# Kernel tuning notes

Hardware: AMD Instinct MI355X
Metric: run time of the kernel (lower is better)

Reference implementation:

```python
import jax, jax.numpy as jnp
import numpy as np

PS = 16            # patch size
STEP = PS - 2      # stride (overlap of 2)
HEADS = 4
DIM = 64
QK = 64
MLP = 128

def _grid(h):
    # static (numpy) row indices of all patch pixels, matching patch_divide's loop
    starts = np.arange(0, h + STEP - PS, STEP)
    tops = np.minimum(starts + PS, h) - PS
    return (tops[:, None] + np.arange(PS)).ravel(), len(starts)

def _div_mask(h):
    # rows/cols covered by two patches get divided by 2 (patch_reverse loops)
    m = np.ones(h, np.float32)
    for i in range(STEP, h + STEP - PS, STEP):
        d = min(i + PS - STEP, h)
        if i < d:
            m[i:d] = 2.0
    return m

def _layernorm(x, g, b):
    mu = x.mean(-1, keepdims=True)
    var = ((x - mu) ** 2).mean(-1, keepdims=True)
    return (x - mu) * jax.lax.rsqrt(var + 1e-5) * g + b

def setup_inputs() -> dict:
    key = jax.random.key(0)
    ks = jax.random.split(key, 8)
    f = lambda k, shp: jax.random.normal(k, shp, jnp.float32) * 0.05
    return {
        "x": jax.random.normal(ks[0], (2, DIM, 226, 226), jnp.float32),
        "ln1_g": jnp.ones((DIM,), jnp.float32), "ln1_b": jnp.zeros((DIM,), jnp.float32),
        "wq": f(ks[1], (DIM, QK)), "wk": f(ks[2], (DIM, QK)), "wv": f(ks[3], (DIM, DIM)),
        "w_proj": f(ks[4], (DIM, DIM)), "b_proj": jnp.zeros((DIM,), jnp.float32),
        "ln2_g": jnp.ones((DIM,), jnp.float32), "ln2_b": jnp.zeros((DIM,), jnp.float32),
        "w_fc1": f(ks[5], (DIM, MLP)), "b_fc1": jnp.zeros((MLP,), jnp.float32),
        "w_dw": f(ks[6], (MLP, 1, 5, 5)), "b_dw": jnp.zeros((MLP,), jnp.float32),
        "w_fc2": f(ks[7], (MLP, DIM)), "b_fc2": jnp.zeros((DIM,), jnp.float32),
    }

def reference(x, ln1_g, ln1_b, wq, wk, wv, w_proj, b_proj,
              ln2_g, ln2_b, w_fc1, b_fc1, w_dw, b_dw, w_fc2, b_fc2):
    b, c, h, w = x.shape
    ri, nh = _grid(h)
    ci, nw = _grid(w)
    n = nh * nw
    # --- patch_divide (vectorized gather of overlapping windows) ---
    p = x[:, :, ri][:, :, :, ci].reshape(b, c, nh, PS, nw, PS)
    t = p.transpose(0, 2, 4, 3, 5, 1).reshape(b * n, PS * PS, c)  # (b n)(h w)c
    # --- PreNorm attention (SDPA default scale = head_dim**-0.5) ---
    y = _layernorm(t, ln1_g, ln1_b)
    dh = QK // HEADS
    q = (y @ wq).reshape(-1, PS * PS, HEADS, dh)
    k = (y @ wk).reshape(-1, PS * PS, HEADS, dh)
    v = (y @ wv).reshape(-1, PS * PS, HEADS, DIM // HEADS)
    logits = jnp.einsum('bqhd,bkhd->bhqk', q, k) * (dh ** -0.5)
    a = jax.nn.softmax(logits, axis=-1)
    o = jnp.einsum('bhqk,bkhd->bqhd', a, v).reshape(-1, PS * PS, DIM)
    t = (o @ w_proj + b_proj) + t
    # --- PreNorm ConvFFN ---
    y = _layernorm(t, ln2_g, ln2_b)
    y = jax.nn.gelu(y @ w_fc1 + b_fc1, approximate=False)
    img = y.reshape(-1, PS, PS, MLP).transpose(0, 3, 1, 2)  # NCHW
    dw = jax.lax.conv_general_dilated(
        img, w_dw, (1, 1), [(2, 2), (2, 2)],
        feature_group_count=MLP,
        dimension_numbers=('NCHW', 'OIHW', 'NCHW')) + b_dw[None, :, None, None]
    dw = jax.nn.gelu(dw, approximate=False).transpose(0, 2, 3, 1).reshape(y.shape)
    y = y + dw
    t = (y @ w_fc2 + b_fc2) + t
    # --- patch_reverse (overlap-add scatter + averaging of double-covered bands) ---
    vals = t.reshape(b, nh, nw, PS, PS, c).transpose(0, 5, 1, 3, 2, 4).reshape(b, c, -1)
    idx = (ri[:, None] * w + ci[None, :]).ravel()
    out = jnp.zeros((b, c, h * w), x.dtype).at[:, :, idx].add(vals)
    out = out.reshape(b, c, h, w) / (_div_mask(h)[:, None] * _div_mask(w)[None, :])
    return out
```

## Files before the change

### kernel.cpp

```cpp
#include <hip/hip_runtime.h>
#include <hip/hip_bf16.h>
#include <math.h>

#define HH 226
#define WW 226
#define HWIMG (226*226)
#define PS 16
#define STP 14
#define TOK 256
#define NPATCH 512
#define NTOK (NPATCH*TOK)
#define OUT_ELEMS (2*64*226*226)

typedef unsigned int u32;
typedef unsigned short u16;
typedef __attribute__((ext_vector_type(8))) short short8;
typedef __attribute__((ext_vector_type(4))) float f32x4;

__device__ __forceinline__ float lo16(u32 u){ return __uint_as_float(u << 16); }
__device__ __forceinline__ float hi16(u32 u){ return __uint_as_float(u & 0xFFFF0000u); }
__device__ __forceinline__ u16 f2bf(float f){
    u32 u = __float_as_uint(f);
    u += 0x7FFFu + ((u >> 16) & 1u);
    return (u16)(u >> 16);
}
__device__ __forceinline__ u32 pack2(float a, float b){
#if defined(__gfx950__) && __has_builtin(__builtin_amdgcn_cvt_pk_bf16_f32)
    auto r = __builtin_amdgcn_cvt_pk_bf16_f32(a, b);
    return *(u32*)&r;
#else
    return (u32)f2bf(a) | ((u32)f2bf(b) << 16);
#endif
}
__device__ __forceinline__ float fexp2(float x){
#if __has_builtin(__builtin_amdgcn_exp2f)
    return __builtin_amdgcn_exp2f(x);
#else
    return exp2f(x);
#endif
}
__device__ __forceinline__ void unpack8(uint4 r, float* d){
    d[0]=lo16(r.x); d[1]=hi16(r.x); d[2]=lo16(r.y); d[3]=hi16(r.y);
    d[4]=lo16(r.z); d[5]=hi16(r.z); d[6]=lo16(r.w); d[7]=hi16(r.w);
}
__device__ __forceinline__ uint4 pack8(const float* a){
    uint4 uu;
    uu.x = pack2(a[0], a[1]);
    uu.y = pack2(a[2], a[3]);
    uu.z = pack2(a[4], a[5]);
    uu.w = pack2(a[6], a[7]);
    return uu;
}
__device__ __forceinline__ float gelu_f(float x){
    return 0.5f * x * (1.0f + erff(x * 0.70710678118654752f));
}

template<int N>
__device__ __forceinline__ void store_bf16(u32* dst, const float* a){
    uint4* p4 = (uint4*)(dst);
    #pragma unroll
    for (int w4 = 0; w4 < N/8; ++w4) p4[w4] = pack8(a + 8*w4);
}

__global__ __launch_bounds__(256, 4) void k0_wt(
    const float* __restrict__ wq, const float* __restrict__ wk,
    const float* __restrict__ wv, u16* __restrict__ wt)
{
    const int i = blockIdx.x*256 + threadIdx.x;
    const int m = i >> 12, rem = i & 4095;
    const int kk = rem >> 6, n = rem & 63;
    const float* w = (m==0 ? wq : (m==1 ? wk : wv));
    wt[m*4096 + n*64 + kk] = f2bf(w[kk*64 + n]);
}

__global__ __launch_bounds__(512, 4) void k1_qkv(
    const float* __restrict__ x, const float* __restrict__ g1, const float* __restrict__ b1,
    const u16* __restrict__ wt,
    float* __restrict__ t_out, u32* __restrict__ qo, u32* __restrict__ ko, u32* __restrict__ vo)
{
    __shared__ u16 ys[256*72];
    __shared__ u32 strip[8][16*34];
    __shared__ float g_s[64], b_s[64];
    const int tid = threadIdx.x;
    if (tid < 64){ g_s[tid]=g1[tid]; b_s[tid]=b1[tid]; }

    const int p = blockIdx.x;
    const int bi = p >> 8, ph = (p >> 4) & 15, pw = p & 15;

    const int tok = tid >> 1, h = tid & 1;
    const int ti = tok >> 4, tj = tok & 15;
    const int r = ph*STP + ti, c = pw*STP + tj;
    const float* xb = x + ((size_t)bi*64 + 32*h)*HWIMG + (size_t)r*WW + c;
    const size_t gtokA = (size_t)p*TOK + tok;
    float* tp = t_out + gtokA*64 + 32*h;

    float v32[32];
    float s1 = 0.f, s2 = 0.f;
    #pragma unroll
    for (int c8 = 0; c8 < 4; ++c8){
        #pragma unroll
        for (int u = 0; u < 8; ++u){
            const float vv = xb[(size_t)(c8*8+u)*HWIMG];
            v32[c8*8+u] = vv;
            s1 += vv; s2 += vv*vv;
        }
        ((float4*)tp)[c8*2]   = make_float4(v32[c8*8+0],v32[c8*8+1],v32[c8*8+2],v32[c8*8+3]);
        ((float4*)tp)[c8*2+1] = make_float4(v32[c8*8+4],v32[c8*8+5],v32[c8*8+6],v32[c8*8+7]);
    }
    s1 += __shfl_xor(s1, 1);
    s2 += __shfl_xor(s2, 1);
    const float mu = s1 * (1.f/64.f);
    const float var = s2 * (1.f/64.f) - mu*mu;
    const float rs = rsqrtf(var + 1e-5f);
    __syncthreads();
    u32* ysw = (u32*)ys;
    #pragma unroll
    for (int i2 = 0; i2 < 16; ++i2){
        const int kk = 32*h + 2*i2;
        const float a0 = (v32[2*i2]  -mu)*rs*g_s[kk]   + b_s[kk];
        const float a1 = (v32[2*i2+1]-mu)*rs*g_s[kk+1] + b_s[kk+1];
        ysw[tok*36 + 16*h + i2] = pack2(a0, a1);
    }
    __syncthreads();

    const int lane = tid & 63;
    const int w8   = tid >> 6;
    const int c15  = lane & 15;
    const int quad = lane >> 4;
    u32* stw = strip[w8];
    const size_t ptok = (size_t)p * TOK;

    for (int mt = 0; mt < 2; ++mt){
        const int T = w8*32 + mt*16;
        short8 af[2];
        #pragma unroll
        for (int kb = 0; kb < 2; ++kb)
            af[kb] = *(const short8*)(ys + (T + c15)*72 + kb*32 + quad*8);

        #pragma unroll
        for (int m = 0; m < 3; ++m){
            short8 bf[2][4];
            #pragma unroll
            for (int kb = 0; kb < 2; ++kb)
                #pragma unroll
                for (int nt = 0; nt < 4; ++nt)
                    bf[kb][nt] = *(const short8*)(wt + m*4096 + (nt*16 + c15)*64 + kb*32 + quad*8);

            f32x4 C[4];
            #pragma unroll
            for (int nt = 0; nt < 4; ++nt) C[nt] = (f32x4){0.f,0.f,0.f,0.f};
            #pragma unroll
            for (int kb = 0; kb < 2; ++kb)
                #pragma unroll
                for (int nt = 0; nt < 4; ++nt)
                    C[nt] = __builtin_amdgcn_mfma_f32_16x16x32_bf16(af[kb], bf[kb][nt], C[nt], 0, 0, 0);

            if (m == 0){
                #pragma unroll
                for (int nt = 0; nt < 4; ++nt)
                    #pragma unroll
                    for (int rr = 0; rr < 4; ++rr)
                        C[nt][rr] *= 0.3606737602222409f;
            }

            #pragma unroll
            for (int nt = 0; nt < 4; ++nt){
                #pragma unroll
                for (int r2 = 0; r2 < 2; ++r2){
                    const float pv0 = __shfl_xor(C[nt][2*r2],   1);
                    const float pv1 = __shfl_xor(C[nt][2*r2+1], 1);
                    u32 wrd; int row;
                    if ((lane & 1) == 0){ wrd = pack2(C[nt][2*r2], pv0);  row = quad*4 + 2*r2; }
                    else                { wrd = pack2(pv1, C[nt][2*r2+1]); row = quad*4 + 2*r2 + 1; }
                    stw[row*34 + nt*8 + (c15 >> 1)] = wrd;
                }
            }

            u32* om = (m==0 ? qo : (m==1 ? ko : vo));
            #pragma unroll
            for (int i = 0; i < 8; ++i){
                const int flat = i*64 + lane;
                const u32 wv = stw[(flat >> 5)*34 + (flat & 31)];
                om[(ptok + T)*32 + flat] = wv;
            }
        }
    }
}

__global__ __launch_bounds__(256, 2) void k2_attn(
    const u16* __restrict__ qg, const u16* __restrict__ kg,
    const u16* __restrict__ vg, u16* __restrict__ og)
{
    __shared__ u16 plds[4][16*280];
    const int tid  = threadIdx.x;
    const int lane = tid & 63;
    const int h    = tid >> 6;
    const int pb   = blockIdx.x;
    const int p    = pb >> 1;
    const int half = pb & 1;
    const int c15  = lane & 15;
    const int quad = lane >> 4;
    const size_t pbase = (size_t)p * TOK * 64;

    short8 kf[16];
    #pragma unroll
    for (int t = 0; t < 16; ++t){
        short8 bf = {0,0,0,0,0,0,0,0};
        if (quad < 2)
            bf = *(const short8*)(kg + pbase + (size_t)(t*16 + c15)*64 + h*16 + quad*8);
        kf[t] = bf;
    }
    short8 vf[8];
    #pragma unroll
    for (int kb = 0; kb < 8; ++kb){
        #pragma unroll
        for (int j = 0; j < 8; ++j)
            vf[kb][j] = (short)vg[pbase + (size_t)(kb*32 + quad*8 + j)*64 + h*16 + c15];
    }
    u16* pw  = &plds[h][0];
    u32* pwq = (u32*)pw + c15*140;

    for (int qi = 0; qi < 8; ++qi){
        const int qt = half*8 + qi;

        short8 qf = {0,0,0,0,0,0,0,0};
        if (quad < 2)
            qf = *(const short8*)(qg + pbase + (size_t)(qt*16 + c15)*64 + h*16 + quad*8);

        f32x4 St[16];
        #pragma unroll
        for (int t = 0; t < 16; ++t){
            f32x4 z = {0.f,0.f,0.f,0.f};
            St[t] = __builtin_amdgcn_mfma_f32_16x16x32_bf16(kf[t], qf, z, 0, 0, 0);
        }

        float rsm[4] = {0.f,0.f,0.f,0.f};
        #pragma unroll
        for (int t = 0; t < 16; ++t){
            #pragma unroll
            for (int r = 0; r < 4; ++r){
                const float pe = fexp2(St[t][r]);
                St[t][r] = pe;
                rsm[r] += pe;
            }
        }
        float s = (rsm[0]+rsm[1]) + (rsm[2]+rsm[3]);
        s += __shfl_xor(s, 16);
        s += __shfl_xor(s, 32);
        const float rinv = __builtin_amdgcn_rcpf(s);
        float rv[4];
        #pragma unroll
        for (int r = 0; r < 4; ++r) rv[r] = __shfl(rinv, quad*4 + r);

        #pragma unroll
        for (int t = 0; t < 16; ++t){
            uint2 wr;
            wr.x = pack2(St[t][0], St[t][1]);
            wr.y = pack2(St[t][2], St[t][3]);
            *(uint2*)(pwq + t*8 + quad*2) = wr;
        }

        f32x4 O0 = {0.f,0.f,0.f,0.f}, O1 = {0.f,0.f,0.f,0.f};
        #pragma unroll
        for (int kb = 0; kb < 4; ++kb){
            const short8 a0 = *(const short8*)(pw + c15*280 + (2*kb)*32 + quad*8);
            const short8 a1 = *(const short8*)(pw + c15*280 + (2*kb+1)*32 + quad*8);
            O0 = __builtin_amdgcn_mfma_f32_16x16x32_bf16(a0, vf[2*kb],   O0, 0, 0, 0);
            O1 = __builtin_amdgcn_mfma_f32_16x16x32_bf16(a1, vf[2*kb+1], O1, 0, 0, 0);
        }

        #pragma unroll
        for (int r = 0; r < 4; ++r){
            const float ov = (O0[r] + O1[r]) * rv[r];
            og[pbase + (size_t)(qt*16 + quad*4 + r)*64 + h*16 + c15] = f2bf(ov);
        }
    }
}

__global__ __launch_bounds__(256, 2) void k3_proj_fc1(
    const u16* __restrict__ og, float* __restrict__ t,
    const float* __restrict__ wp, const float* __restrict__ bp,
    const float* __restrict__ g2, const float* __restrict__ b2,
    const float* __restrict__ wf1, const float* __restrict__ bf1,
    u32* __restrict__ y3)
{
    __shared__ u16 strip[4][16*136];
    __shared__ float bp_s[64], g_s[64], b_s[64], bf_s[128];
    const int tid  = threadIdx.x;
    const int lane = tid & 63;
    const int w    = tid >> 6;
    const int c15  = lane & 15;
    const int quad = lane >> 4;
    if (tid < 64){ bp_s[tid]=bp[tid]; g_s[tid]=g2[tid]; b_s[tid]=b2[tid]; }
    else if (tid >= 128){ const int j = tid - 128; bf_s[j] = bf1[j]; }
    __syncthreads();

    short8 wpf[2][4];
    short8 wff[2][8];
    #pragma unroll
    for (int kb = 0; kb < 2; ++kb){
        #pragma unroll
        for (int nt = 0; nt < 4; ++nt){
            #pragma unroll
            for (int j = 0; j < 8; ++j)
                wpf[kb][nt][j] = (short)f2bf(wp[(kb*32 + quad*8 + j)*64 + nt*16 + c15]);
        }
        #pragma unroll
        for (int nt = 0; nt < 8; ++nt){
            #pragma unroll
            for (int j = 0; j < 8; ++j)
                wff[kb][nt][j] = (short)f2bf(wf1[(kb*32 + quad*8 + j)*128 + nt*16 + c15]);
        }
    }

    const int p = blockIdx.x;
    const size_t pbase = (size_t)p * TOK;
    u16* st = strip[w];
    u32* stw = (u32*)st;

    const float gch[4] = { g_s[0*16+c15], g_s[1*16+c15], g_s[2*16+c15], g_s[3*16+c15] };
    const float bch[4] = { b_s[0*16+c15], b_s[1*16+c15], b_s[2*16+c15], b_s[3*16+c15] };
    const float bpc[4] = { bp_s[0*16+c15], bp_s[1*16+c15], bp_s[2*16+c15], bp_s[3*16+c15] };

    for (int rt = 0; rt < 4; ++rt){
        const int T = w*64 + rt*16;

        short8 af[2];
        #pragma unroll
        for (int kb = 0; kb < 2; ++kb)
            af[kb] = *(const short8*)(og + (pbase + T + c15)*64 + kb*32 + quad*8);

        f32x4 C[4];
        #pragma unroll
        for (int nt = 0; nt < 4; ++nt){
            const float b = bpc[nt];
            C[nt] = (f32x4){b, b, b, b};
        }
        #pragma unroll
        for (int kb = 0; kb < 2; ++kb)
            #pragma unroll
            for (int nt = 0; nt < 4; ++nt)
                C[nt] = __builtin_amdgcn_mfma_f32_16x16x32_bf16(af[kb], wpf[kb][nt], C[nt], 0, 0, 0);

        #pragma unroll
        for (int nt = 0; nt < 4; ++nt){
            #pragma unroll
            for (int r = 0; r < 4; ++r)
                C[nt][r] += t[(pbase + T + quad*4 + r)*64 + nt*16 + c15];
        }
        #pragma unroll
        for (int nt = 0; nt < 4; ++nt){
            #pragma unroll
            for (int r = 0; r < 4; ++r)
                t[(pbase + T + quad*4 + r)*64 + nt*16 + c15] = C[nt][r];
        }

        float rs1[4] = {0,0,0,0}, rs2[4] = {0,0,0,0};
        #pragma unroll
        for (int nt = 0; nt < 4; ++nt)
            #pragma unroll
            for (int r = 0; r < 4; ++r){ rs1[r] += C[nt][r]; rs2[r] += C[nt][r]*C[nt][r]; }
        #pragma unroll
        for (int r = 0; r < 4; ++r){
            rs1[r] += __shfl_xor(rs1[r], 1); rs2[r] += __shfl_xor(rs2[r], 1);
            rs1[r] += __shfl_xor(rs1[r], 2); rs2[r] += __shfl_xor(rs2[r], 2);
            rs1[r] += __shfl_xor(rs1[r], 4); rs2[r] += __shfl_xor(rs2[r], 4);
            rs1[r] += __shfl_xor(rs1[r], 8); rs2[r] += __shfl_xor(rs2[r], 8);
        }
        float muv[4], rsg[4];
        #pragma unroll
        for (int r = 0; r < 4; ++r){
            muv[r] = rs1[r]*(1.f/64.f);
            const float var = rs2[r]*(1.f/64.f) - muv[r]*muv[r];
            rsg[r] = rsqrtf(var + 1e-5f);
        }

        #pragma unroll
        for (int nt = 0; nt < 4; ++nt){
            float yv[4];
            #pragma unroll
            for (int r = 0; r < 4; ++r)
                yv[r] = (C[nt][r]-muv[r])*rsg[r]*gch[nt] + bch[nt];
            #pragma unroll
            for (int r2 = 0; r2 < 2; ++r2){
                const float pv0 = __shfl_xor(yv[2*r2],   1);
                const float pv1 = __shfl_xor(yv[2*r2+1], 1);
                u32 wrd; int row;
                if ((lane & 1) == 0){ wrd = pack2(yv[2*r2], pv0);  row = quad*4 + 2*r2; }
                else                { wrd = pack2(pv1, yv[2*r2+1]); row = quad*4 + 2*r2 + 1; }
                *(u32*)(st + row*136 + nt*16 + (c15 & ~1)) = wrd;
            }
        }

        short8 pa[2];
        #pragma unroll
        for (int kb = 0; kb < 2; ++kb)
            pa[kb] = *(const short8*)(st + c15*136 + kb*32 + quad*8);

        f32x4 F[8];
        #pragma unroll
        for (int nt = 0; nt < 8; ++nt){
            const float b = bf_s[nt*16 + c15];
            F[nt] = (f32x4){b, b, b, b};
        }
        #pragma unroll
        for (int kb = 0; kb < 2; ++kb)
            #pragma unroll
            for (int nt = 0; nt < 8; ++nt)
                F[nt] = __builtin_amdgcn_mfma_f32_16x16x32_bf16(pa[kb], wff[kb][nt], F[nt], 0, 0, 0);

        #pragma unroll
        for (int nt = 0; nt < 8; ++nt)
            #pragma unroll
            for (int r = 0; r < 4; ++r)
                F[nt][r] = gelu_f(F[nt][r]);

        #pragma unroll
        for (int nt = 0; nt < 8; ++nt){
            #pragma unroll
            for (int r2 = 0; r2 < 2; ++r2){
                const float pv0 = __shfl_xor(F[nt][2*r2],   1);
                const float pv1 = __shfl_xor(F[nt][2*r2+1], 1);
                u32 wrd; int row;
                if ((lane & 1) == 0){ wrd = pack2(F[nt][2*r2], pv0);  row = quad*4 + 2*r2; }
                else                { wrd = pack2(pv1, F[nt][2*r2+1]); row = quad*4 + 2*r2 + 1; }
                *(u32*)(st + row*136 + nt*16 + (c15 & ~1)) = wrd;
            }
        }
        #pragma unroll
        for (int i = 0; i < 16; ++i){
            const u32 wv = stw[i*68 + lane];
            y3[(pbase + T + i)*64 + lane] = wv;
        }
    }
}

__global__ __launch_bounds__(256, 2) void k4a_dwconv(
    u32* y3, const float* __restrict__ wdw, const float* __restrict__ bdw)
{
    __shared__ u32 ys[400*33];
    const int tid = threadIdx.x;
    const int p = blockIdx.x;
    const int ch2 = tid & 31;
    const int cg  = tid >> 5;
    const size_t ptok = (size_t)p * TOK;

    const int fti = tid >> 4, ftj = tid & 15;
    const int fstok = (fti+2)*20 + (ftj+2);

    for (int i = tid; i < 13200; i += 256) ys[i] = 0u;

    for (int half = 0; half < 2; ++half){
        __syncthreads();
        {
            const uint4* gp = (const uint4*)(y3 + (ptok + tid)*64 + half*32);
            #pragma unroll
            for (int w = 0; w < 8; ++w){
                uint4 rr = gp[w];
                ys[fstok*33 + w*4+0]=rr.x; ys[fstok*33 + w*4+1]=rr.y;
                ys[fstok*33 + w*4+2]=rr.z; ys[fstok*33 + w*4+3]=rr.w;
            }
        }
        float wA[25], wB[25];
        #pragma unroll
        for (int tap = 0; tap < 25; ++tap){
            wA[tap] = wdw[(half*64 + 2*ch2+0)*25 + tap];
            wB[tap] = wdw[(half*64 + 2*ch2+1)*25 + tap];
        }
        const float bA = bdw[half*64 + 2*ch2+0];
        const float bB = bdw[half*64 + 2*ch2+1];
        __syncthreads();

        #pragma unroll
        for (int cc = 0; cc < 2; ++cc){
            const int c  = cg*2 + cc;
            const int hc = c + 2;
            u32 win[5][5];
            #pragma unroll
            for (int r = 0; r < 4; ++r)
                #pragma unroll
                for (int j = 0; j < 5; ++j)
                    win[r][j] = ys[(r*20 + hc-2+j)*33 + ch2];
            #pragma unroll
            for (int row = 0; row < 16; ++row){
                #pragma unroll
                for (int j = 0; j < 5; ++j)
                    win[(row+4)%5][j] = ys[((row+4)*20 + hc-2+j)*33 + ch2];
                float a0 = bA, a1 = bB;
                #pragma unroll
                for (int di = 0; di < 5; ++di){
                    #pragma unroll
                    for (int dj = 0; dj < 5; ++dj){
                        const u32 v = win[(row+di)%5][dj];
                        a0 += lo16(v)*wA[di*5+dj];
                        a1 += hi16(v)*wB[di*5+dj];
                    }
                }
                const u32 own = win[(row+2)%5][2];
                const float o0 = lo16(own) + gelu_f(a0);
                const float o1 = hi16(own) + gelu_f(a1);
                y3[(ptok + row*16 + c)*64 + half*32 + ch2] = pack2(o0, o1);
            }
        }
    }
}

__global__ __launch_bounds__(256, 2) void k4b_fc2(
    const u16* __restrict__ y3h, const float* __restrict__ t2,
    const float* __restrict__ wf2, const float* __restrict__ bf2,
    float* __restrict__ t3)
{
    const int tid  = threadIdx.x;
    const int lane = tid & 63;
    const int w    = tid >> 6;
    const int c15  = lane & 15;
    const int quad = lane >> 4;

    short8 wf[4][4];
    #pragma unroll
    for (int kb = 0; kb < 4; ++kb)
        #pragma unroll
        for (int nt = 0; nt < 4; ++nt)
            #pragma unroll
            for (int j = 0; j < 8; ++j)
                wf[kb][nt][j] = (short)f2bf(wf2[(kb*32 + quad*8 + j)*64 + nt*16 + c15]);

    float bcc[4];
    #pragma unroll
    for (int nt = 0; nt < 4; ++nt) bcc[nt] = bf2[nt*16 + c15];

    const int p = blockIdx.x;
    const size_t pbase = (size_t)p * TOK;
    float* t3p = t3 + (size_t)p * 16384;

    for (int rt = 0; rt < 4; ++rt){
        const int T = w*64 + rt*16;

        short8 af[4];
        #pragma unroll
        for (int kb = 0; kb < 4; ++kb)
            af[kb] = *(const short8*)(y3h + (pbase + T + c15)*128 + kb*32 + quad*8);

        f32x4 C[4];
        #pragma unroll
        for (int nt = 0; nt < 4; ++nt){
            const float b = bcc[nt];
            C[nt] = (f32x4){b, b, b, b};
        }
        #pragma unroll
        for (int kb = 0; kb < 4; ++kb)
            #pragma unroll
            for (int nt = 0; nt < 4; ++nt)
                C[nt] = __builtin_amdgcn_mfma_f32_16x16x32_bf16(af[kb], wf[kb][nt], C[nt], 0, 0, 0);

        #pragma unroll
        for (int nt = 0; nt < 4; ++nt)
            #pragma unroll
            for (int r = 0; r < 4; ++r)
                C[nt][r] += t2[(pbase + T + quad*4 + r)*64 + nt*16 + c15];

        #pragma unroll
        for (int nt = 0; nt < 4; ++nt)
            #pragma unroll
            for (int r = 0; r < 4; ++r)
                t3p[(nt*16 + c15)*256 + T + quad*4 + r] = C[nt][r];
    }
}

__global__ __launch_bounds__(256, 4) void k5_reverse(
    const float* __restrict__ t3, float* __restrict__ out)
{
    const int e = blockIdx.x*256 + threadIdx.x;
    if (e >= OUT_ELEMS) return;
    const int c = e % WW;
    int tmp = e / WW;
    const int r = tmp % HH;
    tmp /= HH;
    const int ch = tmp & 63;
    const int b = tmp >> 6;
    int pr = r/14; if (pr > 15) pr = 15;
    int pc = c/14; if (pc > 15) pc = 15;
    const int ra = r - pr*14, ca = c - pc*14;
    const int rb = ra + 14, cb = ca + 14;
    const bool hr = (pr >= 1) && (rb < 16);
    const bool hc = (pc >= 1) && (cb < 16);
    #define T3IDX(PH,PC,I,J) (((((b*16+(PH))*16+(PC))*64 + ch) << 8) + (I)*16 + (J))
    float s = t3[T3IDX(pr,pc,ra,ca)];
    if (hr)       s += t3[T3IDX(pr-1,pc,  rb,ca)];
    if (hc)       s += t3[T3IDX(pr,  pc-1,ra,cb)];
    if (hr && hc) s += t3[T3IDX(pr-1,pc-1,rb,cb)];
    const float f = (hr ? 0.5f : 1.f) * (hc ? 0.5f : 1.f);
    out[e] = s * f;
    #undef T3IDX
}

extern "C" void kernel_launch(void* const* d_in, const int* in_sizes, int n_in,
                              void* d_out, int out_size, void* d_ws, size_t ws_size,
                              hipStream_t stream)
{
    const float* x    = (const float*)d_in[0];
    const float* g1   = (const float*)d_in[1];
    const float* b1   = (const float*)d_in[2];
    const float* wq   = (const float*)d_in[3];
    const float* wk   = (const float*)d_in[4];
    const float* wv   = (const float*)d_in[5];
    const float* wp   = (const float*)d_in[6];
    const float* bp   = (const float*)d_in[7];
    const float* g2   = (const float*)d_in[8];
    const float* b2   = (const float*)d_in[9];
    const float* wf1  = (const float*)d_in[10];
    const float* bf1  = (const float*)d_in[11];
    const float* wdw  = (const float*)d_in[12];
    const float* bdw  = (const float*)d_in[13];
    const float* wf2  = (const float*)d_in[14];
    const float* bf2  = (const float*)d_in[15];

    char* ws = (char*)d_ws;
    float* t  = (float*)(ws);
    u32* q    = (u32*)(ws + 33554432);
    u32* k    = (u32*)(ws + 50331648);
    u32* v    = (u32*)(ws + 67108864);
    float* t3 = (float*)(ws + 50331648);
    u32* y3   = (u32*)(ws + 83886080);
    u16* wt   = (u16*)d_out;
    float* out = (float*)d_out;

    k0_wt      <<<48,        256, 0, stream>>>(wq, wk, wv, wt);
    k1_qkv     <<<NPATCH,    512, 0, stream>>>(x, g1, b1, wt, t, q, k, v);
    k2_attn    <<<NPATCH*2,  256, 0, stream>>>((const u16*)q, (const u16*)k, (const u16*)v, (u16*)q);
    k3_proj_fc1<<<NPATCH,    256, 0, stream>>>((const u16*)q, t, wp, bp, g2, b2, wf1, bf1, y3);
    k4a_dwconv <<<NPATCH,    256, 0, stream>>>(y3, wdw, bdw);
    k4b_fc2    <<<NPATCH,    256, 0, stream>>>((const u16*)y3, t, wf2, bf2, t3);
    k5_reverse <<<25538,     256, 0, stream>>>(t3, out);
}
```

Measured before the change: 313.1 us.

## Split QKV kernel into half-patch blocks and store residual channel-major

The QKV kernel now runs two 256-thread blocks per patch instead of one 512-thread block, and block IDs are swizzled so consecutive blocks spread across patches. The residual tensor t is now written and read channel-major per patch ([c][token]), so the writes from the strided x reads coalesce across tokens. The proj/fc1 and fc2 kernels are updated to that layout. This trades the row-major float4 stores for scalar coalesced stores and changes the access pattern in the later kernels' residual reads.

```diff
diff --git a/kernel.cpp b/kernel.cpp
--- a/kernel.cpp
+++ b/kernel.cpp
@@ -55,13 +55,6 @@
     return 0.5f * x * (1.0f + erff(x * 0.70710678118654752f));
 }
 
-template<int N>
-__device__ __forceinline__ void store_bf16(u32* dst, const float* a){
-    uint4* p4 = (uint4*)(dst);
-    #pragma unroll
-    for (int w4 = 0; w4 < N/8; ++w4) p4[w4] = pack8(a + 8*w4);
-}
-
 __global__ __launch_bounds__(256, 4) void k0_wt(
     const float* __restrict__ wq, const float* __restrict__ wk,
     const float* __restrict__ wv, u16* __restrict__ wt)
@@ -73,26 +66,27 @@
     wt[m*4096 + n*64 + kk] = f2bf(w[kk*64 + n]);
 }
 
-__global__ __launch_bounds__(512, 4) void k1_qkv(
+__global__ __launch_bounds__(256, 4) void k1_qkv(
     const float* __restrict__ x, const float* __restrict__ g1, const float* __restrict__ b1,
     const u16* __restrict__ wt,
     float* __restrict__ t_out, u32* __restrict__ qo, u32* __restrict__ ko, u32* __restrict__ vo)
 {
-    __shared__ u16 ys[256*72];
-    __shared__ u32 strip[8][16*34];
+    __shared__ __align__(16) u16 ys[128*72];
+    __shared__ u32 strip[4][16*34];
     __shared__ float g_s[64], b_s[64];
     const int tid = threadIdx.x;
     if (tid < 64){ g_s[tid]=g1[tid]; b_s[tid]=b1[tid]; }
 
-    const int p = blockIdx.x;
+    const int bid = blockIdx.x;
+    const int hp = ((bid & 7) << 7) | (bid >> 3);
+    const int p = hp >> 1, half = hp & 1;
     const int bi = p >> 8, ph = (p >> 4) & 15, pw = p & 15;
 
-    const int tok = tid >> 1, h = tid & 1;
+    const int tokl = tid >> 1, h = tid & 1;
+    const int tok = half*128 + tokl;
     const int ti = tok >> 4, tj = tok & 15;
     const int r = ph*STP + ti, c = pw*STP + tj;
     const float* xb = x + ((size_t)bi*64 + 32*h)*HWIMG + (size_t)r*WW + c;
-    const size_t gtokA = (size_t)p*TOK + tok;
-    float* tp = t_out + gtokA*64 + 32*h;
 
     float v32[32];
     float s1 = 0.f, s2 = 0.f;
@@ -104,8 +98,11 @@
             v32[c8*8+u] = vv;
             s1 += vv; s2 += vv*vv;
         }
-        ((float4*)tp)[c8*2]   = make_float4(v32[c8*8+0],v32[c8*8+1],v32[c8*8+2],v32[c8*8+3]);
-        ((float4*)tp)[c8*2+1] = make_float4(v32[c8*8+4],v32[c8*8+5],v32[c8*8+6],v32[c8*8+7]);
+    }
+    {
+        float* tp = t_out + (size_t)p*16384 + (size_t)(32*h)*256 + tok;
+        #pragma unroll
+        for (int cc = 0; cc < 32; ++cc) tp[cc*256] = v32[cc];
     }
     s1 += __shfl_xor(s1, 1);
     s2 += __shfl_xor(s2, 1);
@@ -119,23 +116,24 @@
         const int kk = 32*h + 2*i2;
         const float a0 = (v32[2*i2]  -mu)*rs*g_s[kk]   + b_s[kk];
         const float a1 = (v32[2*i2+1]-mu)*rs*g_s[kk+1] + b_s[kk+1];
-        ysw[tok*36 + 16*h + i2] = pack2(a0, a1);
+        ysw[tokl*36 + 16*h + i2] = pack2(a0, a1);
     }
     __syncthreads();
 
     const int lane = tid & 63;
-    const int w8   = tid >> 6;
+    const int w4   = tid >> 6;
     const int c15  = lane & 15;
     const int quad = lane >> 4;
-    u32* stw = strip[w8];
+    u32* stw = strip[w4];
     const size_t ptok = (size_t)p * TOK;
 
     for (int mt = 0; mt < 2; ++mt){
-        const int T = w8*32 + mt*16;
+        const int Tl = w4*32 + mt*16;
+        const int T  = half*128 + Tl;
         short8 af[2];
         #pragma unroll
         for (int kb = 0; kb < 2; ++kb)
-            af[kb] = *(const short8*)(ys + (T + c15)*72 + kb*32 + quad*8);
+            af[kb] = *(const short8*)(ys + (Tl + c15)*72 + kb*32 + quad*8);
 
         #pragma unroll
         for (int m = 0; m < 3; ++m){
@@ -315,6 +313,7 @@
 
     const int p = blockIdx.x;
     const size_t pbase = (size_t)p * TOK;
+    float* tch = t + (size_t)p * 16384;
     u16* st = strip[w];
     u32* stw = (u32*)st;
 
@@ -346,13 +345,13 @@
         for (int nt = 0; nt < 4; ++nt){
             #pragma unroll
             for (int r = 0; r < 4; ++r)
-                C[nt][r] += t[(pbase + T + quad*4 + r)*64 + nt*16 + c15];
+                C[nt][r] += tch[(nt*16 + c15)*256 + T + quad*4 + r];
         }
         #pragma unroll
         for (int nt = 0; nt < 4; ++nt){
             #pragma unroll
             for (int r = 0; r < 4; ++r)
-                t[(pbase + T + quad*4 + r)*64 + nt*16 + c15] = C[nt][r];
+                tch[(nt*16 + c15)*256 + T + quad*4 + r] = C[nt][r];
         }
 
         float rs1[4] = {0,0,0,0}, rs2[4] = {0,0,0,0};
@@ -531,6 +530,7 @@
 
     const int p = blockIdx.x;
     const size_t pbase = (size_t)p * TOK;
+    const float* t2p = t2 + (size_t)p * 16384;
     float* t3p = t3 + (size_t)p * 16384;
 
     for (int rt = 0; rt < 4; ++rt){
@@ -557,7 +557,7 @@
         for (int nt = 0; nt < 4; ++nt)
             #pragma unroll
             for (int r = 0; r < 4; ++r)
-                C[nt][r] += t2[(pbase + T + quad*4 + r)*64 + nt*16 + c15];
+                C[nt][r] += t2p[(nt*16 + c15)*256 + T + quad*4 + r];
 
         #pragma unroll
         for (int nt = 0; nt < 4; ++nt)
@@ -626,7 +626,7 @@
     float* out = (float*)d_out;
 
     k0_wt      <<<48,        256, 0, stream>>>(wq, wk, wv, wt);
-    k1_qkv     <<<NPATCH,    512, 0, stream>>>(x, g1, b1, wt, t, q, k, v);
+    k1_qkv     <<<NPATCH*2,  256, 0, stream>>>(x, g1, b1, wt, t, q, k, v);
     k2_attn    <<<NPATCH*2,  256, 0, stream>>>((const u16*)q, (const u16*)k, (const u16*)v, (u16*)q);
     k3_proj_fc1<<<NPATCH,    256, 0, stream>>>((const u16*)q, t, wp, bp, g2, b2, wf1, bf1, y3);
     k4a_dwconv <<<NPATCH,    256, 0, stream>>>(y3, wdw, bdw);
```

Measured after the change: 305.9 us. 1.02x faster.
